# Kernel tuning notes

Hardware: AMD Instinct MI355X
Metric: run time of the kernel (lower is better)

Reference implementation:

```python
import jax, jax.numpy as jnp
import numpy as np

LEAK = 0.2

def setup_inputs() -> dict:
    key = jax.random.key(0)
    ks = jax.random.split(key, 8)
    B, D, H1, H2, F = 2048, 3072, 512, 256, 100
    s = lambda fan_in: 1.0 / np.sqrt(fan_in)
    return {
        "x":  jax.random.normal(ks[0], (B, D), dtype=jnp.float32),
        "W1": jax.random.uniform(ks[1], (D, H1), jnp.float32, -s(D), s(D)),
        "b1": jnp.zeros((H1,), jnp.float32),
        "W2": jax.random.uniform(ks[2], (H1, H2), jnp.float32, -s(H1), s(H1)),
        "b2": jnp.zeros((H2,), jnp.float32),
        "T":  jax.random.normal(ks[3], (H2, F), dtype=jnp.float32),
        "Wf": jax.random.uniform(ks[4], (H2 + F, 1), jnp.float32, -s(H2 + F), s(H2 + F)),
        "bf": jnp.zeros((1,), jnp.float32),
    }

def reference(x, W1, b1, W2, b2, T, Wf, bf):
    # MLP stack with LeakyReLU(0.2)
    h = jax.nn.leaky_relu(x @ W1 + b1, LEAK)          # (B,512)
    h = jax.nn.leaky_relu(h @ W2 + b2, LEAK)          # (B,256)
    # Minibatch discrimination: pairwise L1 per feature, exp, sum over batch
    m = h @ T                                          # (B,100)
    d = jnp.abs(m[:, None, :] - m[None, :, :])         # (B,B,100)
    feats = jnp.sum(jnp.exp(-d), axis=1)               # (B,100)
    z = jnp.concatenate([h, feats], axis=1)            # (B,356)
    return z @ Wf + bf                                 # (B,1)
```

## Files before the change

### kernel.cpp

```cpp
#include <hip/hip_runtime.h>
#include <hip/hip_bf16.h>

#define LEAK 0.2f

typedef __attribute__((ext_vector_type(8))) short short8;
typedef __attribute__((ext_vector_type(4))) float f32x4;

__global__ __launch_bounds__(256) void k_convert(const float* __restrict__ x,
                                                 __hip_bfloat16* __restrict__ xb, int n4) {
  int idx = blockIdx.x * 256 + threadIdx.x;
  if (idx >= n4) return;
  float4 v = reinterpret_cast<const float4*>(x)[idx];
  union { ushort4 u; __hip_bfloat16 h[4]; } c;
  c.h[0] = __float2bfloat16(v.x);
  c.h[1] = __float2bfloat16(v.y);
  c.h[2] = __float2bfloat16(v.z);
  c.h[3] = __float2bfloat16(v.w);
  reinterpret_cast<ushort4*>(xb)[idx] = c.u;
}

__global__ __launch_bounds__(256) void k_transpose(const float* __restrict__ W,
                                                   __hip_bfloat16* __restrict__ Wt,
                                                   int K, int N) {
  __shared__ float tile[32][33];
  int k0 = blockIdx.x * 32, n0 = blockIdx.y * 32;
  int tx = threadIdx.x, ty = threadIdx.y;
#pragma unroll
  for (int r = 0; r < 4; ++r) {
    int k = k0 + ty + r * 8;
    int n = n0 + tx;
    tile[ty + r * 8][tx] = (n < N) ? W[(long)k * N + n] : 0.f;
  }
  __syncthreads();
#pragma unroll
  for (int r = 0; r < 4; ++r) {
    int n = n0 + ty + r * 8;
    int k = k0 + tx;
    Wt[(long)n * K + k] = __float2bfloat16(tile[tx][ty + r * 8]);
  }
}

template <bool TRANSP>
__global__ __launch_bounds__(256) void k_gemm(const __hip_bfloat16* __restrict__ A,
                                              const __hip_bfloat16* __restrict__ Bt,
                                              float* __restrict__ Cp,
                                              int M, int N, int K, int KSPL, int ldO) {
  __shared__ __align__(16) __hip_bfloat16 As[64][40];
  __shared__ __align__(16) __hip_bfloat16 Bs[64][40];
  int tid = threadIdx.x;
  int lane = tid & 63;
  int wv = tid >> 6;
  int wm = wv & 1, wn = wv >> 1;
  int quad = lane >> 4, l16 = lane & 15;
  long m0 = (long)blockIdx.x * 64, n0 = (long)blockIdx.y * 64;
  int srow = tid >> 2, scol = (tid & 3) * 8;
  int kStart = blockIdx.z * KSPL;
  const __hip_bfloat16* Ag = A + (m0 + srow) * K + kStart + scol;
  const __hip_bfloat16* Bg = Bt + (n0 + srow) * K + kStart + scol;

  int4 ra = *reinterpret_cast<const int4*>(Ag);
  int4 rb = *reinterpret_cast<const int4*>(Bg);

  f32x4 acc[2][2] = {};
  for (int kb = 0; kb < KSPL; kb += 32) {
    *reinterpret_cast<int4*>(&As[srow][scol]) = ra;
    *reinterpret_cast<int4*>(&Bs[srow][scol]) = rb;
    __syncthreads();
    if (kb + 32 < KSPL) {
      ra = *reinterpret_cast<const int4*>(Ag + kb + 32);
      rb = *reinterpret_cast<const int4*>(Bg + kb + 32);
    }
    short8 af[2], bfr[2];
#pragma unroll
    for (int t = 0; t < 2; ++t) {
      af[t]  = *reinterpret_cast<const short8*>(&As[wm * 32 + t * 16 + l16][quad * 8]);
      bfr[t] = *reinterpret_cast<const short8*>(&Bs[wn * 32 + t * 16 + l16][quad * 8]);
    }
#pragma unroll
    for (int tm = 0; tm < 2; ++tm)
#pragma unroll
      for (int tn = 0; tn < 2; ++tn)
        acc[tm][tn] =
            __builtin_amdgcn_mfma_f32_16x16x32_bf16(af[tm], bfr[tn], acc[tm][tn], 0, 0, 0);
    __syncthreads();
  }

  float* Cz = Cp + (long)blockIdx.z * M * N;
#pragma unroll
  for (int tm = 0; tm < 2; ++tm)
#pragma unroll
    for (int tn = 0; tn < 2; ++tn)
#pragma unroll
      for (int r = 0; r < 4; ++r) {
        long gm = m0 + wm * 32 + tm * 16 + quad * 4 + r;
        long gn = n0 + wn * 32 + tn * 16 + l16;
        if (TRANSP) Cz[gn * ldO + gm] = acc[tm][tn][r];
        else        Cz[gm * ldO + gn] = acc[tm][tn][r];
      }
}

template <int NZ, bool OUTF>
__global__ __launch_bounds__(256) void k_comb(const float* __restrict__ P,
                                              const float* __restrict__ bias,
                                              float* __restrict__ Of,
                                              __hip_bfloat16* __restrict__ Ob,
                                              int total4, int nmask) {
  int idx = blockIdx.x * 256 + threadIdx.x;
  if (idx >= total4) return;
  float4 v = reinterpret_cast<const float4*>(P)[idx];
#pragma unroll
  for (int z = 1; z < NZ; ++z) {
    float4 a = reinterpret_cast<const float4*>(P + (long)z * total4 * 4)[idx];
    v.x += a.x; v.y += a.y; v.z += a.z; v.w += a.w;
  }
  int col = (idx * 4) & nmask;
  float4 bs = *reinterpret_cast<const float4*>(bias + col);
  v.x += bs.x; v.y += bs.y; v.z += bs.z; v.w += bs.w;
  v.x = v.x > 0.f ? v.x : LEAK * v.x;
  v.y = v.y > 0.f ? v.y : LEAK * v.y;
  v.z = v.z > 0.f ? v.z : LEAK * v.z;
  v.w = v.w > 0.f ? v.w : LEAK * v.w;
  if (OUTF) reinterpret_cast<float4*>(Of)[idx] = v;
  union { ushort4 u; __hip_bfloat16 h[4]; } c;
  c.h[0] = __float2bfloat16(v.x);
  c.h[1] = __float2bfloat16(v.y);
  c.h[2] = __float2bfloat16(v.z);
  c.h[3] = __float2bfloat16(v.w);
  reinterpret_cast<ushort4*>(Ob)[idx] = c.u;
}

__global__ __launch_bounds__(1024) void k_bucketfeats(const float* __restrict__ mTz,
                                                      float* __restrict__ featsT) {
  __shared__ float sP[2048], sN[2048];
  __shared__ float Sp[2048], Sn[2048];
  __shared__ int Smeta[2048];
  __shared__ short sB[2048];
  __shared__ int cnt[256], bstart[256], bcur[256];
  __shared__ float bsP[256], bsN[256], Pbel[256], Nab[256];
  __shared__ float wred[32];
  __shared__ float sMin, sMax;
  int f = blockIdx.x;
  int t = threadIdx.x;
  int lane = t & 63, wv = t >> 6;
  const long FS = 2048L * 128;
  const float* row = mTz + (long)f * 2048;

  float m[2];
  float lmin = 3.4e38f, lmax = -3.4e38f;
#pragma unroll
  for (int r = 0; r < 2; ++r) {
    int e = t + r * 1024;
    float v = row[e] + row[FS + e] + row[2 * FS + e] + row[3 * FS + e];
    m[r] = v;
    lmin = fminf(lmin, v);
    lmax = fmaxf(lmax, v);
  }
#pragma unroll
  for (int d = 32; d; d >>= 1) {
    lmin = fminf(lmin, __shfl_down(lmin, d));
    lmax = fmaxf(lmax, __shfl_down(lmax, d));
  }
  if (lane == 0) { wred[wv] = lmin; wred[16 + wv] = lmax; }
  if (t < 256) cnt[t] = 0;
  __syncthreads();
  if (t == 0) {
    float a = wred[0], b = wred[16];
    for (int i = 1; i < 16; ++i) { a = fminf(a, wred[i]); b = fmaxf(b, wred[16 + i]); }
    sMin = a; sMax = b;
  }
  __syncthreads();
  float mn = sMin, mx = sMax;
  float rge = mx - mn;
  float scale = (rge > 1e-20f) ? 255.0f / rge : 0.f;
  float mid = 0.5f * (mn + mx);
#pragma unroll
  for (int r = 0; r < 2; ++r) {
    int e = t + r * 1024;
    float v = m[r];
    int b = (int)((v - mn) * scale);
    b = b < 255 ? b : 255;
    float arg = fminf(fmaxf(v - mid, -60.f), 60.f);
    sP[e] = __expf(arg);
    sN[e] = __expf(-arg);
    sB[e] = (short)b;
    atomicAdd(&cnt[b], 1);
  }
  __syncthreads();
  if (wv == 0) {
    int b4 = lane * 4;
    int c0 = cnt[b4], c1 = cnt[b4 + 1], c2 = cnt[b4 + 2], c3 = cnt[b4 + 3];
    int tot = c0 + c1 + c2 + c3;
    int inc = tot;
#pragma unroll
    for (int d = 1; d < 64; d <<= 1) {
      int y = __shfl_up(inc, d);
      if (lane >= d) inc += y;
    }
    int run = inc - tot;
    bstart[b4] = run; bcur[b4] = run; run += c0;
    bstart[b4 + 1] = run; bcur[b4 + 1] = run; run += c1;
    bstart[b4 + 2] = run; bcur[b4 + 2] = run; run += c2;
    bstart[b4 + 3] = run; bcur[b4 + 3] = run;
  }
  __syncthreads();
#pragma unroll
  for (int r = 0; r < 2; ++r) {
    int e = t + r * 1024;
    int b = sB[e];
    int slot = atomicAdd(&bcur[b], 1);
    Sp[slot] = sP[e];
    Sn[slot] = sN[e];
    Smeta[slot] = (b << 16) | e;
  }
  __syncthreads();
  if (t < 256) {
    int s0 = bstart[t], s1 = s0 + cnt[t];
    float ap = 0.f, an = 0.f;
    for (int q = s0; q < s1; ++q) { ap += Sp[q]; an += Sn[q]; }
    bsP[t] = ap; bsN[t] = an;
  }
  __syncthreads();
  if (wv == 0) {
    int b4 = lane * 4;
    float p0 = bsP[b4], p1 = bsP[b4 + 1], p2 = bsP[b4 + 2], p3 = bsP[b4 + 3];
    float n0 = bsN[b4], n1 = bsN[b4 + 1], n2 = bsN[b4 + 2], n3 = bsN[b4 + 3];
    float tp = p0 + p1 + p2 + p3, tn = n0 + n1 + n2 + n3;
    float ip = tp, in_ = tn;
#pragma unroll
    for (int d = 1; d < 64; d <<= 1) {
      float yp = __shfl_up(ip, d);
      float yn = __shfl_up(in_, d);
      if (lane >= d) { ip += yp; in_ += yn; }
    }
    float totn = __shfl(in_, 63);
    float runp = ip - tp;
    float runn = in_ - tn;
    Pbel[b4] = runp; Nab[b4] = totn - runn - n0; runp += p0; runn += n0;
    Pbel[b4 + 1] = runp; Nab[b4 + 1] = totn - runn - n1; runp += p1; runn += n1;
    Pbel[b4 + 2] = runp; Nab[b4 + 2] = totn - runn - n2; runp += p2; runn += n2;
    Pbel[b4 + 3] = runp; Nab[b4 + 3] = totn - runn - n3;
  }
  __syncthreads();
#pragma unroll
  for (int r = 0; r < 2; ++r) {
    int s = t + r * 1024;
    int meta = Smeta[s];
    int b = meta >> 16;
    int idx = meta & 0xFFFF;
    float p = Sp[s], n = Sn[s];
    float acc = n * Pbel[b] + p * Nab[b];
    int q0 = bstart[b], q1 = q0 + cnt[b];
    for (int q = q0; q < q1; ++q) acc += fminf(p * Sn[q], n * Sp[q]);
    featsT[(long)f * 2048 + idx] = acc;
  }
}

__global__ __launch_bounds__(256) void k_final(const float* __restrict__ h2f,
                                               const float* __restrict__ featsT,
                                               const float* __restrict__ Wf,
                                               const float* __restrict__ bfp,
                                               float* __restrict__ out) {
  int wv = threadIdx.x >> 6, lane = threadIdx.x & 63;
  long i = (long)blockIdx.x * 4 + wv;
  const float* hrow = h2f + i * 256;
  float s = 0.f;
#pragma unroll
  for (int c = lane; c < 256; c += 64) s += hrow[c] * Wf[c];
  for (int f = lane; f < 100; f += 64) s += featsT[(long)f * 2048 + i] * Wf[256 + f];
#pragma unroll
  for (int off = 32; off; off >>= 1) s += __shfl_down(s, off);
  if (lane == 0) out[i] = s + bfp[0];
}

extern "C" void kernel_launch(void* const* d_in, const int* in_sizes, int n_in,
                              void* d_out, int out_size, void* d_ws, size_t ws_size,
                              hipStream_t stream) {
  const float* x  = (const float*)d_in[0];
  const float* W1 = (const float*)d_in[1];
  const float* b1 = (const float*)d_in[2];
  const float* W2 = (const float*)d_in[3];
  const float* b2 = (const float*)d_in[4];
  const float* T  = (const float*)d_in[5];
  const float* Wf = (const float*)d_in[6];
  const float* bf = (const float*)d_in[7];
  float* out = (float*)d_out;

  char* w = (char*)d_ws;
  auto alloc = [&](size_t b) { char* p = w; w += (b + 255) & ~(size_t)255; return p; };
  char*           xbr  = alloc(2048L * 3072 * 2);
  __hip_bfloat16* xb   = (__hip_bfloat16*)xbr;
  float*          P2   = (float*)xbr;
  float*          P3   = (float*)(xbr + 4194304);
  float*          feT  = (float*)(xbr + 8388608);
  __hip_bfloat16* W1t  = (__hip_bfloat16*)alloc(512L * 3072 * 2);
  __hip_bfloat16* W2t  = (__hip_bfloat16*)alloc(256L * 512 * 2);
  __hip_bfloat16* Tt   = (__hip_bfloat16*)alloc(128L * 256 * 2);
  __hip_bfloat16* h1b  = (__hip_bfloat16*)alloc(2048L * 512 * 2);
  float*          h2f  = (float*)alloc(2048L * 256 * 4);
  __hip_bfloat16* h2b  = (__hip_bfloat16*)alloc(2048L * 256 * 2);
  float*          P1   = (float*)alloc(3L * 2048 * 512 * 4);

  k_convert<<<6144, 256, 0, stream>>>(x, xb, 1572864);
  k_transpose<<<dim3(96, 16), dim3(32, 8), 0, stream>>>(W1, W1t, 3072, 512);
  k_transpose<<<dim3(16, 8),  dim3(32, 8), 0, stream>>>(W2, W2t, 512, 256);
  k_transpose<<<dim3(8, 4),   dim3(32, 8), 0, stream>>>(T,  Tt,  256, 100);
  k_gemm<false><<<dim3(32, 8, 3), 256, 0, stream>>>(xb, W1t, P1, 2048, 512, 3072, 1024, 512);
  k_comb<3, false><<<1024, 256, 0, stream>>>(P1, b1, nullptr, h1b, 262144, 511);
  k_gemm<false><<<dim3(32, 4, 2), 256, 0, stream>>>(h1b, W2t, P2, 2048, 256, 512, 256, 256);
  k_comb<2, true><<<512, 256, 0, stream>>>(P2, b2, h2f, h2b, 131072, 255);
  k_gemm<true><<<dim3(32, 2, 4), 256, 0, stream>>>(h2b, Tt, P3, 2048, 128, 256, 64, 2048);
  k_bucketfeats<<<100, 1024, 0, stream>>>(P3, feT);
  k_final<<<512, 256, 0, stream>>>(h2f, feT, Wf, bf, out);
}
```

Baseline: 138.1 us.

## Fuse prep kernels, async LDS-loaded GEMM tiles, fold T projection into feats

Merges the convert and transpose kernels into one launch. GEMM1 moves to 128x128 tiles with a double-buffered global_load_lds pipeline. GEMM2 gains a fused bias and LeakyReLU epilogue that writes bf16, removing its combine kernel. The h2·T projection is computed inside the features kernel with scalar FMAs from bf16 h2 instead of through a separate MFMA GEMM and split-K buffers, and the final kernel reads bf16 h2. This cuts launches and intermediate traffic, but leaves a scalar dot product in the features kernel and slightly lowers precision in the final dot product.

```diff
diff --git a/kernel.cpp b/kernel.cpp
--- a/kernel.cpp
+++ b/kernel.cpp
@@ -6,103 +6,150 @@
 typedef __attribute__((ext_vector_type(8))) short short8;
 typedef __attribute__((ext_vector_type(4))) float f32x4;
 
-__global__ __launch_bounds__(256) void k_convert(const float* __restrict__ x,
-                                                 __hip_bfloat16* __restrict__ xb, int n4) {
-  int idx = blockIdx.x * 256 + threadIdx.x;
-  if (idx >= n4) return;
-  float4 v = reinterpret_cast<const float4*>(x)[idx];
-  union { ushort4 u; __hip_bfloat16 h[4]; } c;
-  c.h[0] = __float2bfloat16(v.x);
-  c.h[1] = __float2bfloat16(v.y);
-  c.h[2] = __float2bfloat16(v.z);
-  c.h[3] = __float2bfloat16(v.w);
-  reinterpret_cast<ushort4*>(xb)[idx] = c.u;
-}
-
-__global__ __launch_bounds__(256) void k_transpose(const float* __restrict__ W,
-                                                   __hip_bfloat16* __restrict__ Wt,
-                                                   int K, int N) {
+__device__ __forceinline__ float bf2f(unsigned short u) {
+  union { unsigned v; float f; } c;
+  c.v = ((unsigned)u) << 16;
+  return c.f;
+}
+
+__device__ __forceinline__ void gll16(const void* g, void* l) {
+  __builtin_amdgcn_global_load_lds((const __attribute__((address_space(1))) void*)g,
+                                   (__attribute__((address_space(3))) void*)l, 16, 0, 0);
+}
+
+__global__ __launch_bounds__(256) void k_prep(const float* __restrict__ x,
+                                              __hip_bfloat16* __restrict__ xb,
+                                              const float* __restrict__ W1,
+                                              __hip_bfloat16* __restrict__ W1t,
+                                              const float* __restrict__ W2,
+                                              __hip_bfloat16* __restrict__ W2t) {
+  int b = blockIdx.x;
+  int t = threadIdx.x;
+  if (b < 6144) {
+    int idx = b * 256 + t;
+    float4 v = reinterpret_cast<const float4*>(x)[idx];
+    union { ushort4 u; __hip_bfloat16 h[4]; } c;
+    c.h[0] = __float2bfloat16(v.x);
+    c.h[1] = __float2bfloat16(v.y);
+    c.h[2] = __float2bfloat16(v.z);
+    c.h[3] = __float2bfloat16(v.w);
+    reinterpret_cast<ushort4*>(xb)[idx] = c.u;
+    return;
+  }
   __shared__ float tile[32][33];
-  int k0 = blockIdx.x * 32, n0 = blockIdx.y * 32;
-  int tx = threadIdx.x, ty = threadIdx.y;
-#pragma unroll
-  for (int r = 0; r < 4; ++r) {
-    int k = k0 + ty + r * 8;
-    int n = n0 + tx;
-    tile[ty + r * 8][tx] = (n < N) ? W[(long)k * N + n] : 0.f;
-  }
-  __syncthreads();
-#pragma unroll
-  for (int r = 0; r < 4; ++r) {
-    int n = n0 + ty + r * 8;
-    int k = k0 + tx;
-    Wt[(long)n * K + k] = __float2bfloat16(tile[tx][ty + r * 8]);
-  }
-}
-
-template <bool TRANSP>
+  const float* W;
+  __hip_bfloat16* Wt;
+  int K, N, kblk, nblk;
+  if (b < 7680) {
+    int bb = b - 6144;
+    W = W1; Wt = W1t; K = 3072; N = 512;
+    kblk = bb % 96; nblk = bb / 96;
+  } else {
+    int bb = b - 7680;
+    W = W2; Wt = W2t; K = 512; N = 256;
+    kblk = bb % 16; nblk = bb / 16;
+  }
+  int k0 = kblk * 32, n0 = nblk * 32;
+  int tx = t & 31, ty = t >> 5;
+#pragma unroll
+  for (int r = 0; r < 4; ++r)
+    tile[ty + r * 8][tx] = W[(long)(k0 + ty + r * 8) * N + n0 + tx];
+  __syncthreads();
+#pragma unroll
+  for (int r = 0; r < 4; ++r)
+    Wt[(long)(n0 + ty + r * 8) * K + k0 + tx] = __float2bfloat16(tile[tx][ty + r * 8]);
+}
+
+template <int TM, int TN, bool FUSE>
 __global__ __launch_bounds__(256) void k_gemm(const __hip_bfloat16* __restrict__ A,
                                               const __hip_bfloat16* __restrict__ Bt,
+                                              const float* __restrict__ bias,
                                               float* __restrict__ Cp,
-                                              int M, int N, int K, int KSPL, int ldO) {
-  __shared__ __align__(16) __hip_bfloat16 As[64][40];
-  __shared__ __align__(16) __hip_bfloat16 Bs[64][40];
+                                              __hip_bfloat16* __restrict__ Cb,
+                                              int M, int N, int K, int KSPL) {
+  constexpr int BM = 32 * TM, BN = 32 * TN;
+  constexpr int CA = BM / 64, CB = BN / 64;
+  __shared__ __align__(16) __hip_bfloat16 As[2][BM * 32];
+  __shared__ __align__(16) __hip_bfloat16 Bs[2][BN * 32];
   int tid = threadIdx.x;
   int lane = tid & 63;
   int wv = tid >> 6;
   int wm = wv & 1, wn = wv >> 1;
   int quad = lane >> 4, l16 = lane & 15;
-  long m0 = (long)blockIdx.x * 64, n0 = (long)blockIdx.y * 64;
-  int srow = tid >> 2, scol = (tid & 3) * 8;
+  long m0 = (long)blockIdx.x * BM, n0 = (long)blockIdx.y * BN;
   int kStart = blockIdx.z * KSPL;
-  const __hip_bfloat16* Ag = A + (m0 + srow) * K + kStart + scol;
-  const __hip_bfloat16* Bg = Bt + (n0 + srow) * K + kStart + scol;
-
-  int4 ra = *reinterpret_cast<const int4*>(Ag);
-  int4 rb = *reinterpret_cast<const int4*>(Bg);
-
-  f32x4 acc[2][2] = {};
-  for (int kb = 0; kb < KSPL; kb += 32) {
-    *reinterpret_cast<int4*>(&As[srow][scol]) = ra;
-    *reinterpret_cast<int4*>(&Bs[srow][scol]) = rb;
+  int lrow = lane >> 2, lcol = (lane & 3) * 8;
+
+  const __hip_bfloat16* Ap[CA];
+  const __hip_bfloat16* Bp[CB];
+#pragma unroll
+  for (int c = 0; c < CA; ++c)
+    Ap[c] = A + (m0 + (wv * CA + c) * 16 + lrow) * (long)K + kStart + lcol;
+#pragma unroll
+  for (int c = 0; c < CB; ++c)
+    Bp[c] = Bt + (n0 + (wv * CB + c) * 16 + lrow) * (long)K + kStart + lcol;
+
+  auto stage = [&](int buf, int kb) {
+#pragma unroll
+    for (int c = 0; c < CA; ++c)
+      gll16(Ap[c] + kb, &As[buf][(wv * CA + c) * 512]);
+#pragma unroll
+    for (int c = 0; c < CB; ++c)
+      gll16(Bp[c] + kb, &Bs[buf][(wv * CB + c) * 512]);
+  };
+
+  f32x4 acc[TM][TN] = {};
+  stage(0, 0);
+  int nIter = KSPL >> 5;
+  for (int it = 0; it < nIter; ++it) {
     __syncthreads();
-    if (kb + 32 < KSPL) {
-      ra = *reinterpret_cast<const int4*>(Ag + kb + 32);
-      rb = *reinterpret_cast<const int4*>(Bg + kb + 32);
-    }
-    short8 af[2], bfr[2];
-#pragma unroll
-    for (int t = 0; t < 2; ++t) {
-      af[t]  = *reinterpret_cast<const short8*>(&As[wm * 32 + t * 16 + l16][quad * 8]);
-      bfr[t] = *reinterpret_cast<const short8*>(&Bs[wn * 32 + t * 16 + l16][quad * 8]);
-    }
-#pragma unroll
-    for (int tm = 0; tm < 2; ++tm)
-#pragma unroll
-      for (int tn = 0; tn < 2; ++tn)
-        acc[tm][tn] =
-            __builtin_amdgcn_mfma_f32_16x16x32_bf16(af[tm], bfr[tn], acc[tm][tn], 0, 0, 0);
-    __syncthreads();
-  }
-
-  float* Cz = Cp + (long)blockIdx.z * M * N;
-#pragma unroll
-  for (int tm = 0; tm < 2; ++tm)
-#pragma unroll
-    for (int tn = 0; tn < 2; ++tn)
-#pragma unroll
-      for (int r = 0; r < 4; ++r) {
-        long gm = m0 + wm * 32 + tm * 16 + quad * 4 + r;
-        long gn = n0 + wn * 32 + tn * 16 + l16;
-        if (TRANSP) Cz[gn * ldO + gm] = acc[tm][tn][r];
-        else        Cz[gm * ldO + gn] = acc[tm][tn][r];
-      }
-}
-
-template <int NZ, bool OUTF>
+    if (it + 1 < nIter) stage((it + 1) & 1, (it + 1) * 32);
+    int buf = it & 1;
+    short8 af[TM], bfg[TN];
+#pragma unroll
+    for (int t = 0; t < TM; ++t)
+      af[t] = *reinterpret_cast<const short8*>(&As[buf][(wm * 16 * TM + t * 16 + l16) * 32 + quad * 8]);
+#pragma unroll
+    for (int u = 0; u < TN; ++u)
+      bfg[u] = *reinterpret_cast<const short8*>(&Bs[buf][(wn * 16 * TN + u * 16 + l16) * 32 + quad * 8]);
+#pragma unroll
+    for (int t = 0; t < TM; ++t)
+#pragma unroll
+      for (int u = 0; u < TN; ++u)
+        acc[t][u] = __builtin_amdgcn_mfma_f32_16x16x32_bf16(af[t], bfg[u], acc[t][u], 0, 0, 0);
+  }
+
+  if (FUSE) {
+#pragma unroll
+    for (int t = 0; t < TM; ++t)
+#pragma unroll
+      for (int u = 0; u < TN; ++u)
+#pragma unroll
+        for (int r = 0; r < 4; ++r) {
+          long gm = m0 + wm * 16 * TM + t * 16 + quad * 4 + r;
+          long gn = n0 + wn * 16 * TN + u * 16 + l16;
+          float v = acc[t][u][r] + bias[gn];
+          v = v > 0.f ? v : LEAK * v;
+          Cb[gm * N + gn] = __float2bfloat16(v);
+        }
+  } else {
+    float* Cz = Cp + (long)blockIdx.z * M * N;
+#pragma unroll
+    for (int t = 0; t < TM; ++t)
+#pragma unroll
+      for (int u = 0; u < TN; ++u)
+#pragma unroll
+        for (int r = 0; r < 4; ++r) {
+          long gm = m0 + wm * 16 * TM + t * 16 + quad * 4 + r;
+          long gn = n0 + wn * 16 * TN + u * 16 + l16;
+          Cz[gm * N + gn] = acc[t][u][r];
+        }
+  }
+}
+
+template <int NZ>
 __global__ __launch_bounds__(256) void k_comb(const float* __restrict__ P,
                                               const float* __restrict__ bias,
-                                              float* __restrict__ Of,
                                               __hip_bfloat16* __restrict__ Ob,
                                               int total4, int nmask) {
   int idx = blockIdx.x * 256 + threadIdx.x;
@@ -120,7 +167,6 @@
   v.y = v.y > 0.f ? v.y : LEAK * v.y;
   v.z = v.z > 0.f ? v.z : LEAK * v.z;
   v.w = v.w > 0.f ? v.w : LEAK * v.w;
-  if (OUTF) reinterpret_cast<float4*>(Of)[idx] = v;
   union { ushort4 u; __hip_bfloat16 h[4]; } c;
   c.h[0] = __float2bfloat16(v.x);
   c.h[1] = __float2bfloat16(v.y);
@@ -129,8 +175,10 @@
   reinterpret_cast<ushort4*>(Ob)[idx] = c.u;
 }
 
-__global__ __launch_bounds__(1024) void k_bucketfeats(const float* __restrict__ mTz,
-                                                      float* __restrict__ featsT) {
+__global__ __launch_bounds__(1024) void k_feats(const __hip_bfloat16* __restrict__ h2b,
+                                                const float* __restrict__ T,
+                                                float* __restrict__ featsT) {
+  __shared__ float Tcol[256];
   __shared__ float sP[2048], sN[2048];
   __shared__ float Sp[2048], Sn[2048];
   __shared__ int Smeta[2048];
@@ -142,18 +190,28 @@
   int f = blockIdx.x;
   int t = threadIdx.x;
   int lane = t & 63, wv = t >> 6;
-  const long FS = 2048L * 128;
-  const float* row = mTz + (long)f * 2048;
+
+  if (t < 256) Tcol[t] = T[t * 100 + f];
+  if (t < 256) cnt[t] = 0;
+  __syncthreads();
 
   float m[2];
   float lmin = 3.4e38f, lmax = -3.4e38f;
 #pragma unroll
   for (int r = 0; r < 2; ++r) {
     int e = t + r * 1024;
-    float v = row[e] + row[FS + e] + row[2 * FS + e] + row[3 * FS + e];
-    m[r] = v;
-    lmin = fminf(lmin, v);
-    lmax = fmaxf(lmax, v);
+    const short8* hp = reinterpret_cast<const short8*>(h2b + (long)e * 256);
+    float acc = 0.f;
+#pragma unroll 4
+    for (int c8 = 0; c8 < 32; ++c8) {
+      short8 hv = hp[c8];
+#pragma unroll
+      for (int j = 0; j < 8; ++j)
+        acc += bf2f((unsigned short)hv[j]) * Tcol[c8 * 8 + j];
+    }
+    m[r] = acc;
+    lmin = fminf(lmin, acc);
+    lmax = fmaxf(lmax, acc);
   }
 #pragma unroll
   for (int d = 32; d; d >>= 1) {
@@ -161,7 +219,6 @@
     lmax = fmaxf(lmax, __shfl_down(lmax, d));
   }
   if (lane == 0) { wred[wv] = lmin; wred[16 + wv] = lmax; }
-  if (t < 256) cnt[t] = 0;
   __syncthreads();
   if (t == 0) {
     float a = wred[0], b = wred[16];
@@ -255,17 +312,17 @@
   }
 }
 
-__global__ __launch_bounds__(256) void k_final(const float* __restrict__ h2f,
+__global__ __launch_bounds__(256) void k_final(const __hip_bfloat16* __restrict__ h2b,
                                                const float* __restrict__ featsT,
                                                const float* __restrict__ Wf,
                                                const float* __restrict__ bfp,
                                                float* __restrict__ out) {
   int wv = threadIdx.x >> 6, lane = threadIdx.x & 63;
   long i = (long)blockIdx.x * 4 + wv;
-  const float* hrow = h2f + i * 256;
+  const unsigned short* hrow = reinterpret_cast<const unsigned short*>(h2b) + i * 256;
   float s = 0.f;
 #pragma unroll
-  for (int c = lane; c < 256; c += 64) s += hrow[c] * Wf[c];
+  for (int c = lane; c < 256; c += 64) s += bf2f(hrow[c]) * Wf[c];
   for (int f = lane; f < 100; f += 64) s += featsT[(long)f * 2048 + i] * Wf[256 + f];
 #pragma unroll
   for (int off = 32; off; off >>= 1) s += __shfl_down(s, off);
@@ -287,28 +344,20 @@
 
   char* w = (char*)d_ws;
   auto alloc = [&](size_t b) { char* p = w; w += (b + 255) & ~(size_t)255; return p; };
-  char*           xbr  = alloc(2048L * 3072 * 2);
-  __hip_bfloat16* xb   = (__hip_bfloat16*)xbr;
-  float*          P2   = (float*)xbr;
-  float*          P3   = (float*)(xbr + 4194304);
-  float*          feT  = (float*)(xbr + 8388608);
-  __hip_bfloat16* W1t  = (__hip_bfloat16*)alloc(512L * 3072 * 2);
-  __hip_bfloat16* W2t  = (__hip_bfloat16*)alloc(256L * 512 * 2);
-  __hip_bfloat16* Tt   = (__hip_bfloat16*)alloc(128L * 256 * 2);
-  __hip_bfloat16* h1b  = (__hip_bfloat16*)alloc(2048L * 512 * 2);
-  float*          h2f  = (float*)alloc(2048L * 256 * 4);
-  __hip_bfloat16* h2b  = (__hip_bfloat16*)alloc(2048L * 256 * 2);
-  float*          P1   = (float*)alloc(3L * 2048 * 512 * 4);
-
-  k_convert<<<6144, 256, 0, stream>>>(x, xb, 1572864);
-  k_transpose<<<dim3(96, 16), dim3(32, 8), 0, stream>>>(W1, W1t, 3072, 512);
-  k_transpose<<<dim3(16, 8),  dim3(32, 8), 0, stream>>>(W2, W2t, 512, 256);
-  k_transpose<<<dim3(8, 4),   dim3(32, 8), 0, stream>>>(T,  Tt,  256, 100);
-  k_gemm<false><<<dim3(32, 8, 3), 256, 0, stream>>>(xb, W1t, P1, 2048, 512, 3072, 1024, 512);
-  k_comb<3, false><<<1024, 256, 0, stream>>>(P1, b1, nullptr, h1b, 262144, 511);
-  k_gemm<false><<<dim3(32, 4, 2), 256, 0, stream>>>(h1b, W2t, P2, 2048, 256, 512, 256, 256);
-  k_comb<2, true><<<512, 256, 0, stream>>>(P2, b2, h2f, h2b, 131072, 255);
-  k_gemm<true><<<dim3(32, 2, 4), 256, 0, stream>>>(h2b, Tt, P3, 2048, 128, 256, 64, 2048);
-  k_bucketfeats<<<100, 1024, 0, stream>>>(P3, feT);
-  k_final<<<512, 256, 0, stream>>>(h2f, feT, Wf, bf, out);
-}
+  __hip_bfloat16* xb  = (__hip_bfloat16*)alloc(2048L * 3072 * 2);
+  __hip_bfloat16* W1t = (__hip_bfloat16*)alloc(512L * 3072 * 2);
+  __hip_bfloat16* W2t = (__hip_bfloat16*)alloc(256L * 512 * 2);
+  __hip_bfloat16* h1b = (__hip_bfloat16*)alloc(2048L * 512 * 2);
+  __hip_bfloat16* h2b = (__hip_bfloat16*)alloc(2048L * 256 * 2);
+  float*          feT = (float*)alloc(100L * 2048 * 4);
+  float*          P1  = (float*)alloc(4L * 2048 * 512 * 4);
+
+  k_prep<<<7808, 256, 0, stream>>>(x, xb, W1, W1t, W2, W2t);
+  k_gemm<4, 4, false><<<dim3(16, 4, 4), 256, 0, stream>>>(
+      xb, W1t, nullptr, P1, nullptr, 2048, 512, 3072, 768);
+  k_comb<4><<<1024, 256, 0, stream>>>(P1, b1, h1b, 262144, 511);
+  k_gemm<2, 2, true><<<dim3(32, 4, 1), 256, 0, stream>>>(
+      h1b, W2t, b2, nullptr, h2b, 2048, 256, 512, 512);
+  k_feats<<<100, 1024, 0, stream>>>(h2b, T, feT);
+  k_final<<<512, 256, 0, stream>>>(h2b, feT, Wf, bf, out);
+}
```

Result: slower. 158.1 us (+14.5%).
